# Kernel optimization log

Measured on AMD Instinct MI355X. Metric: run time of the kernel, lower is better.

Reference implementation:

```python
import jax, jax.numpy as jnp
import numpy as np

N = 50000   # nodes
E = 800000  # directed edges
D = 128     # input_channels


def _kaiming(key, shape):
    fan_in = shape[0]
    return jax.random.normal(key, shape, jnp.float32) * np.float32(np.sqrt(2.0 / fan_in))


def setup_inputs():
    key = jax.random.key(0)
    ks = jax.random.split(key, 8)
    x = jax.random.normal(ks[0], (N, D), jnp.float32)
    edge_index = jax.random.randint(ks[1], (2, E), 0, N, dtype=jnp.int32)
    return {
        "x": x,
        "edge_index": edge_index,
        "W_in": _kaiming(ks[2], (D, D)),      "b_in": jnp.zeros((D,), jnp.float32),
        "W1": _kaiming(ks[3], (D, 2 * D)),    "b1": jnp.zeros((2 * D,), jnp.float32),
        "W2": _kaiming(ks[4], (2 * D, D)),    "b2": jnp.zeros((D,), jnp.float32),
        "W3": _kaiming(ks[5], (D, D // 2)),   "b3": jnp.zeros((D // 2,), jnp.float32),
        "W_out": _kaiming(ks[6], (D // 2, 1)), "b_out": jnp.zeros((1,), jnp.float32),
    }


def _gcn_conv(x, src, dst, W, b, n):
    """PyG GCNConv: add self-loops, symmetric D^-1/2 (A+I) D^-1/2 normalization."""
    h = x @ W  # [n, out]
    loop = jnp.arange(n, dtype=src.dtype)
    s = jnp.concatenate([src, loop])  # message sources (x_j)
    d = jnp.concatenate([dst, loop])  # aggregation targets (x_i)
    deg = jax.ops.segment_sum(jnp.ones_like(d, jnp.float32), d, num_segments=n)
    dis = jnp.where(deg > 0, jax.lax.rsqrt(jnp.maximum(deg, 1.0)), 0.0)
    norm = dis[s] * dis[d]  # [E+n]
    msg = h[s] * norm[:, None]  # gather + scale
    out = jax.ops.segment_sum(msg, d, num_segments=n)  # scatter-add
    return out + b


def reference(x, edge_index, W_in, b_in, W1, b1, W2, b2, W3, b3, W_out, b_out):
    src, dst = edge_index[0], edge_index[1]
    n = x.shape[0]
    lrelu = lambda t: jax.nn.leaky_relu(t, 0.01)
    # dropout in eval mode (identity)
    h = lrelu(x @ W_in + b_in)
    h = lrelu(_gcn_conv(h, src, dst, W1, b1, n))
    h = lrelu(_gcn_conv(h, src, dst, W2, b2, n))
    h = lrelu(_gcn_conv(h, src, dst, W3, b3, n))
    return h @ W_out + b_out  # [n, 1]
```

## Files before the change

### kernel.cpp

```cpp
#include <hip/hip_runtime.h>


#define LRELU(v) ((v) > 0.f ? (v) : 0.01f * (v))

typedef __attribute__((ext_vector_type(8))) _Float16 half8;
typedef __attribute__((ext_vector_type(8))) float float8;
typedef __attribute__((ext_vector_type(4))) float floatx4;

constexpr int CAP = 64;

__global__ __launch_bounds__(256) void k_prep(const int* __restrict__ src,
                                              const int* __restrict__ dst,
                                              int* __restrict__ cnt,
                                              unsigned short* __restrict__ pad,
                                              const float* __restrict__ W_in,
                                              const float* __restrict__ W1,
                                              const float* __restrict__ W2,
                                              const float* __restrict__ W3,
                                              _Float16* __restrict__ wt_in,
                                              _Float16* __restrict__ wt1,
                                              _Float16* __restrict__ wt2,
                                              _Float16* __restrict__ wt3,
                                              int E, int PR) {
  const int b = blockIdx.x;
  const int tid = threadIdx.x;
  if (b < 128) {
    const int m = b >> 5;
    const int blk = b & 31;
    const int idx = blk * 256 + tid;
    if (m == 0) {
      for (int i = idx; i < 128 * 128; i += 8192) {
        const int k = i >> 7, f = i & 127;
        wt_in[f * 128 + k] = (_Float16)W_in[i];
      }
    } else if (m == 1) {
      for (int i = idx; i < 128 * 256; i += 8192) {
        const int k = i >> 8, f = i & 255;
        wt1[f * 128 + k] = (_Float16)W1[i];
      }
    } else if (m == 2) {
      for (int i = idx; i < 256 * 128; i += 8192) {
        const int k = i >> 7, f = i & 127;
        wt2[f * 256 + k] = (_Float16)W2[i];
      }
    } else {
      for (int i = idx; i < 128 * 64; i += 8192) {
        const int k = i >> 6, f = i & 63;
        wt3[f * 128 + k] = (_Float16)W3[i];
      }
    }
  } else {
    const int bb = b - 128;
    const int range = bb & 7;
    const int chunk = bb >> 3;
    const int e = chunk * 256 + tid;
    if (e < E) {
      const int d = dst[e];
      if (d / PR == range) {
        const int pos = atomicAdd(&cnt[d], 1);
        if (pos < CAP) pad[(long)d * CAP + pos] = (unsigned short)src[e];
      }
    }
  }
}

template <int K, int F, int EPI, typename IT>
__global__ __launch_bounds__(256) void k_gemm(const IT* __restrict__ X,
                                              const _Float16* __restrict__ Wt,
                                              const float* __restrict__ b,
                                              const int* __restrict__ cnt,
                                              _Float16* __restrict__ out, int M) {
  constexpr int TM = 64;
  constexpr int PAD = 8;
  constexpr int LK = K + PAD;
  constexpr int CW = F / 4;
  constexpr int NT = CW / 16;
  constexpr int NK = K / 32;
  __shared__ _Float16 xs[TM * LK];

  const int m0 = blockIdx.x * TM;
  const int tid = threadIdx.x;
  const int w = tid >> 6;
  const int lane = tid & 63;
  const int m = lane & 15;
  const int q = lane >> 4;

  half8 breg[NT][NK];
#pragma unroll
  for (int t = 0; t < NT; ++t)
#pragma unroll
    for (int kc = 0; kc < NK; ++kc)
      breg[t][kc] =
          *(const half8*)&Wt[(long)(w * CW + t * 16 + m) * K + kc * 32 + q * 8];

  constexpr int CPR = K / 8;
  for (int idx = tid; idx < TM * CPR; idx += 256) {
    const int row = idx / CPR;
    const int kk = idx % CPR;
    const int g = m0 + row;
    half8 h = (half8)(_Float16)0.f;
    if (g < M) {
      if constexpr (sizeof(IT) == 4) {
        const float4* p = (const float4*)&X[(long)g * K + kk * 8];
        float4 a = p[0], c = p[1];
        h[0] = (_Float16)a.x; h[1] = (_Float16)a.y;
        h[2] = (_Float16)a.z; h[3] = (_Float16)a.w;
        h[4] = (_Float16)c.x; h[5] = (_Float16)c.y;
        h[6] = (_Float16)c.z; h[7] = (_Float16)c.w;
      } else {
        h = *(const half8*)&X[(long)g * K + kk * 8];
      }
    }
    *(half8*)&xs[row * LK + kk * 8] = h;
  }
  __syncthreads();

  floatx4 acc[4][NT];
#pragma unroll
  for (int rt = 0; rt < 4; ++rt)
#pragma unroll
    for (int t = 0; t < NT; ++t) acc[rt][t] = (floatx4){0.f, 0.f, 0.f, 0.f};

#pragma unroll
  for (int kc = 0; kc < NK; ++kc) {
    half8 af[4];
#pragma unroll
    for (int rt = 0; rt < 4; ++rt)
      af[rt] = *(const half8*)&xs[(rt * 16 + m) * LK + kc * 32 + q * 8];
#pragma unroll
    for (int rt = 0; rt < 4; ++rt)
#pragma unroll
      for (int t = 0; t < NT; ++t)
        acc[rt][t] = __builtin_amdgcn_mfma_f32_16x16x32_f16(af[rt], breg[t][kc],
                                                            acc[rt][t], 0, 0, 0);
  }

#pragma unroll
  for (int rt = 0; rt < 4; ++rt) {
#pragma unroll
    for (int r = 0; r < 4; ++r) {
      const int row = m0 + rt * 16 + q * 4 + r;
      if (row < M) {
        const float dv = rsqrtf((float)cnt[row] + 1.0f);
#pragma unroll
        for (int t = 0; t < NT; ++t) {
          const int col = w * CW + t * 16 + m;
          float v = acc[rt][t][r];
          if constexpr (EPI == 0) { v += b[col]; v = LRELU(v); v *= dv; }
          if constexpr (EPI == 2) { v *= dv; }
          out[(long)row * F + col] = (_Float16)v;
        }
      }
    }
  }
}

__global__ __launch_bounds__(256) void k_gemm2x(const _Float16* __restrict__ X,
                                                const _Float16* __restrict__ Wt1,
                                                const float* __restrict__ b1,
                                                const _Float16* __restrict__ Wt2,
                                                const int* __restrict__ cnt,
                                                _Float16* __restrict__ out,
                                                int M) {
  constexpr int TM = 64;
  constexpr int LK1 = 128 + 8;
  constexpr int LK2 = 256 + 8;
  __shared__ _Float16 xs[TM * LK1];
  __shared__ _Float16 ys[TM * LK2];

  const int m0 = blockIdx.x * TM;
  const int tid = threadIdx.x;
  const int w = tid >> 6;
  const int lane = tid & 63;
  const int m = lane & 15;
  const int q = lane >> 4;

  for (int idx = tid; idx < TM * 16; idx += 256) {
    const int row = idx >> 4;
    const int kk = idx & 15;
    const int g = m0 + row;
    half8 h = (half8)(_Float16)0.f;
    if (g < M) h = *(const half8*)&X[(long)g * 128 + kk * 8];
    *(half8*)&xs[row * LK1 + kk * 8] = h;
  }

  half8 breg1[4][4];
#pragma unroll
  for (int t = 0; t < 4; ++t)
#pragma unroll
    for (int kc = 0; kc < 4; ++kc)
      breg1[t][kc] =
          *(const half8*)&Wt1[(long)(w * 64 + t * 16 + m) * 128 + kc * 32 + q * 8];

  __syncthreads();

  floatx4 acc1[4][4];
#pragma unroll
  for (int rt = 0; rt < 4; ++rt)
#pragma unroll
    for (int t = 0; t < 4; ++t) acc1[rt][t] = (floatx4){0.f, 0.f, 0.f, 0.f};

#pragma unroll
  for (int kc = 0; kc < 4; ++kc) {
    half8 af[4];
#pragma unroll
    for (int rt = 0; rt < 4; ++rt)
      af[rt] = *(const half8*)&xs[(rt * 16 + m) * LK1 + kc * 32 + q * 8];
#pragma unroll
    for (int rt = 0; rt < 4; ++rt)
#pragma unroll
      for (int t = 0; t < 4; ++t)
        acc1[rt][t] = __builtin_amdgcn_mfma_f32_16x16x32_f16(af[rt], breg1[t][kc],
                                                             acc1[rt][t], 0, 0, 0);
  }

#pragma unroll
  for (int rt = 0; rt < 4; ++rt) {
#pragma unroll
    for (int r = 0; r < 4; ++r) {
      const int row = rt * 16 + q * 4 + r;
#pragma unroll
      for (int t = 0; t < 4; ++t) {
        const int col = w * 64 + t * 16 + m;
        float v = acc1[rt][t][r] + b1[col];
        ys[row * LK2 + col] = (_Float16)LRELU(v);
      }
    }
  }

  half8 breg2[2][8];
#pragma unroll
  for (int t = 0; t < 2; ++t)
#pragma unroll
    for (int kc = 0; kc < 8; ++kc)
      breg2[t][kc] =
          *(const half8*)&Wt2[(long)(w * 32 + t * 16 + m) * 256 + kc * 32 + q * 8];

  __syncthreads();

  floatx4 acc2[4][2];
#pragma unroll
  for (int rt = 0; rt < 4; ++rt)
#pragma unroll
    for (int t = 0; t < 2; ++t) acc2[rt][t] = (floatx4){0.f, 0.f, 0.f, 0.f};

#pragma unroll
  for (int kc = 0; kc < 8; ++kc) {
    half8 af[4];
#pragma unroll
    for (int rt = 0; rt < 4; ++rt)
      af[rt] = *(const half8*)&ys[(rt * 16 + m) * LK2 + kc * 32 + q * 8];
#pragma unroll
    for (int rt = 0; rt < 4; ++rt)
#pragma unroll
      for (int t = 0; t < 2; ++t)
        acc2[rt][t] = __builtin_amdgcn_mfma_f32_16x16x32_f16(af[rt], breg2[t][kc],
                                                             acc2[rt][t], 0, 0, 0);
  }

#pragma unroll
  for (int rt = 0; rt < 4; ++rt) {
#pragma unroll
    for (int r = 0; r < 4; ++r) {
      const int row = m0 + rt * 16 + q * 4 + r;
      if (row < M) {
        const float dv = rsqrtf((float)cnt[row] + 1.0f);
#pragma unroll
        for (int t = 0; t < 2; ++t) {
          const int col = w * 32 + t * 16 + m;
          out[(long)row * 128 + col] = (_Float16)(acc2[rt][t][r] * dv);
        }
      }
    }
  }
}

template <int F, int MODE>
__global__ __launch_bounds__(256) void k_agg(const _Float16* __restrict__ G,
                                             const unsigned short* __restrict__ pad,
                                             const int* __restrict__ cnt,
                                             const float* __restrict__ b,
                                             const float* __restrict__ Wout,
                                             const float* __restrict__ bout,
                                             void* __restrict__ out, int N) {
  const int w = threadIdx.x >> 6;
  const int lane = threadIdx.x & 63;
  const int c = lane & 7;
  const int j = lane >> 3;
  const int n = j >> 2;
  const int jj = j & 3;
  const int i0 = blockIdx.x * 8 + w * 2;
  int i = i0 + n;
  const bool valid = (i < N);
  if (!valid) i = N - 1;
  const int col0 = (F == 128) ? ((int)blockIdx.y << 6) : 0;

  const _Float16* gbase = G + col0 + c * 8;
  const int cn = min(cnt[i], CAP);
  const unsigned short* plist = pad + (long)i * CAP;

  float8 acc = {0.f, 0.f, 0.f, 0.f, 0.f, 0.f, 0.f, 0.f};
  if (jj == 0)
    acc = __builtin_convertvector(*(const half8*)(gbase + (long)i * F), float8);
  for (int e = jj; e < cn; e += 4) {
    const int s = plist[e];
    acc += __builtin_convertvector(*(const half8*)(gbase + (long)s * F), float8);
  }
#pragma unroll
  for (int k = 0; k < 8; ++k) {
    acc[k] += __shfl_xor(acc[k], 8);
    acc[k] += __shfl_xor(acc[k], 16);
  }

  const float dv = rsqrtf((float)cnt[i] + 1.0f);
  if constexpr (MODE == 2) {
    float p = 0.f;
#pragma unroll
    for (int k = 0; k < 8; ++k) {
      const int col = c * 8 + k;
      float v = acc[k] * dv + b[col];
      v = LRELU(v);
      p += v * Wout[col];
    }
    p += __shfl_xor(p, 1);
    p += __shfl_xor(p, 2);
    p += __shfl_xor(p, 4);
    if (valid && jj == 0 && c == 0) ((float*)out)[i] = p + bout[0];
  } else {
    if (valid && jj == 0) {
      half8 hv;
#pragma unroll
      for (int k = 0; k < 8; ++k) {
        float v = acc[k] * dv;
        if constexpr (MODE == 1) { v += b[col0 + c * 8 + k]; v = LRELU(v); }
        hv[k] = (_Float16)v;
      }
      *(half8*)&((_Float16*)out)[(long)i * F + col0 + c * 8] = hv;
    }
  }
}


extern "C" void kernel_launch(void* const* d_in, const int* in_sizes, int n_in,
                              void* d_out, int out_size, void* d_ws, size_t ws_size,
                              hipStream_t stream) {
  const float* x     = (const float*)d_in[0];
  const int* eidx    = (const int*)d_in[1];
  const float* W_in  = (const float*)d_in[2];
  const float* b_in  = (const float*)d_in[3];
  const float* W1    = (const float*)d_in[4];
  const float* b1    = (const float*)d_in[5];
  const float* W2    = (const float*)d_in[6];
  const float* b2    = (const float*)d_in[7];
  const float* W3    = (const float*)d_in[8];
  const float* b3    = (const float*)d_in[9];
  const float* W_out = (const float*)d_in[10];
  const float* b_out = (const float*)d_in[11];
  float* out = (float*)d_out;

  const int N = in_sizes[0] / 128;
  const int E = in_sizes[1] / 2;
  const int* src = eidx;
  const int* dst = eidx + E;
  const int PR = (N + 7) / 8;

  size_t off = 0;
  char* base = (char*)d_ws;
  auto alloc = [&](size_t bytes) -> void* {
    void* p = base + off;
    off = (off + bytes + 255) & ~(size_t)255;
    return p;
  };
  int* cnt            = (int*)alloc((size_t)N * sizeof(int));
  unsigned short* pad = (unsigned short*)alloc((size_t)N * CAP * 2);
  _Float16* wt_in     = (_Float16*)alloc((size_t)128 * 128 * 2);
  _Float16* wt1       = (_Float16*)alloc((size_t)256 * 128 * 2);
  _Float16* wt2       = (_Float16*)alloc((size_t)128 * 256 * 2);
  _Float16* wt3       = (_Float16*)alloc((size_t)64 * 128 * 2);
  _Float16* buf1      = (_Float16*)alloc((size_t)N * 128 * 2);
  _Float16* buf2      = (_Float16*)alloc((size_t)N * 128 * 2);
  _Float16* buf3      = (_Float16*)alloc((size_t)N * 64 * 2);

  hipMemsetAsync(cnt, 0, (size_t)N * sizeof(int), stream);

  const int gE = (E + 255) / 256;
  const int gRows = (N + 63) / 64;
  const int gAggP = (N + 7) / 8;

  k_prep<<<128 + 8 * gE, 256, 0, stream>>>(src, dst, cnt, pad,
                                           W_in, W1, W2, W3,
                                           wt_in, wt1, wt2, wt3, E, PR);

  k_gemm<128, 128, 0, float><<<gRows, 256, 0, stream>>>(x, wt_in, b_in, cnt,
                                                        buf1, N);
  k_agg<128, 0><<<dim3(gAggP, 2), 256, 0, stream>>>(buf1, pad, cnt, nullptr,
                                                    nullptr, nullptr, buf2, N);
  k_gemm2x<<<gRows, 256, 0, stream>>>(buf2, wt1, b1, wt2, cnt, buf1, N);
  k_agg<128, 1><<<dim3(gAggP, 2), 256, 0, stream>>>(buf1, pad, cnt, b2,
                                                    nullptr, nullptr, buf2, N);
  k_gemm<128, 64, 2, _Float16><<<gRows, 256, 0, stream>>>(buf2, wt3, nullptr,
                                                          cnt, buf3, N);
  k_agg<64, 2><<<gAggP, 256, 0, stream>>>(buf3, pad, cnt, b3,
                                          W_out, b_out, out, N);
}
```

Before: 273.8 us.

## Fuse all GCN stages into one persistent cooperative kernel with grid syncs

Replaces the memset and seven separate kernel launches with a single cooperative persistent kernel that loops over tiles and separates the phases with grid-wide barriers. Weight conversion, count zeroing, edge bucketing, the GEMMs and the aggregations all run inside it, and the old multi-kernel path stays as a fallback. The aim is to remove launch gaps and tail effects between the small stages. In exchange, the grid is capped by occupancy, which limits latency hiding in the gather-bound aggregation, grid.sync adds its own cost, and gemm2x now reuses one shared buffer with an extra barrier.

```diff
diff --git a/kernel.cpp b/kernel.cpp
--- a/kernel.cpp
+++ b/kernel.cpp
@@ -1,4 +1,7 @@
 #include <hip/hip_runtime.h>
+#include <hip/hip_cooperative_groups.h>
+
+namespace cg = cooperative_groups;
 
 
 #define LRELU(v) ((v) > 0.f ? (v) : 0.01f * (v))
@@ -8,6 +11,360 @@
 typedef __attribute__((ext_vector_type(4))) float floatx4;
 
 constexpr int CAP = 64;
+constexpr int SMEM_H = 16896;
+
+template <int K, int F, int EPI, typename IT>
+__device__ void phase_gemm(const IT* __restrict__ X,
+                           const _Float16* __restrict__ Wt,
+                           const float* __restrict__ b,
+                           const int* __restrict__ cnt,
+                           _Float16* __restrict__ out, int M,
+                           _Float16* xs) {
+  constexpr int TM = 64;
+  constexpr int LK = K + 8;
+  constexpr int CW = F / 4;
+  constexpr int NT = CW / 16;
+  constexpr int NK = K / 32;
+
+  const int tid = threadIdx.x;
+  const int w = tid >> 6;
+  const int lane = tid & 63;
+  const int m = lane & 15;
+  const int q = lane >> 4;
+  const int nTiles = (M + TM - 1) / TM;
+
+  half8 breg[NT][NK];
+#pragma unroll
+  for (int t = 0; t < NT; ++t)
+#pragma unroll
+    for (int kc = 0; kc < NK; ++kc)
+      breg[t][kc] =
+          *(const half8*)&Wt[(long)(w * CW + t * 16 + m) * K + kc * 32 + q * 8];
+
+  for (int tile = blockIdx.x; tile < nTiles; tile += gridDim.x) {
+    const int m0 = tile * TM;
+    __syncthreads();
+    constexpr int CPR = K / 8;
+    for (int idx = tid; idx < TM * CPR; idx += 256) {
+      const int row = idx / CPR;
+      const int kk = idx % CPR;
+      const int g = m0 + row;
+      half8 h = (half8)(_Float16)0.f;
+      if (g < M) {
+        if constexpr (sizeof(IT) == 4) {
+          const float4* p = (const float4*)&X[(long)g * K + kk * 8];
+          float4 a = p[0], c = p[1];
+          h[0] = (_Float16)a.x; h[1] = (_Float16)a.y;
+          h[2] = (_Float16)a.z; h[3] = (_Float16)a.w;
+          h[4] = (_Float16)c.x; h[5] = (_Float16)c.y;
+          h[6] = (_Float16)c.z; h[7] = (_Float16)c.w;
+        } else {
+          h = *(const half8*)&X[(long)g * K + kk * 8];
+        }
+      }
+      *(half8*)&xs[row * LK + kk * 8] = h;
+    }
+    __syncthreads();
+
+    floatx4 acc[4][NT];
+#pragma unroll
+    for (int rt = 0; rt < 4; ++rt)
+#pragma unroll
+      for (int t = 0; t < NT; ++t) acc[rt][t] = (floatx4){0.f, 0.f, 0.f, 0.f};
+
+#pragma unroll
+    for (int kc = 0; kc < NK; ++kc) {
+      half8 af[4];
+#pragma unroll
+      for (int rt = 0; rt < 4; ++rt)
+        af[rt] = *(const half8*)&xs[(rt * 16 + m) * LK + kc * 32 + q * 8];
+#pragma unroll
+      for (int rt = 0; rt < 4; ++rt)
+#pragma unroll
+        for (int t = 0; t < NT; ++t)
+          acc[rt][t] = __builtin_amdgcn_mfma_f32_16x16x32_f16(
+              af[rt], breg[t][kc], acc[rt][t], 0, 0, 0);
+    }
+
+#pragma unroll
+    for (int rt = 0; rt < 4; ++rt) {
+#pragma unroll
+      for (int r = 0; r < 4; ++r) {
+        const int row = m0 + rt * 16 + q * 4 + r;
+        if (row < M) {
+          const float dv = rsqrtf((float)cnt[row] + 1.0f);
+#pragma unroll
+          for (int t = 0; t < NT; ++t) {
+            const int col = w * CW + t * 16 + m;
+            float v = acc[rt][t][r];
+            if constexpr (EPI == 0) { v += b[col]; v = LRELU(v); v *= dv; }
+            if constexpr (EPI == 2) { v *= dv; }
+            out[(long)row * F + col] = (_Float16)v;
+          }
+        }
+      }
+    }
+  }
+}
+
+__device__ void phase_gemm2x(const _Float16* __restrict__ X,
+                             const _Float16* __restrict__ Wt1,
+                             const float* __restrict__ b1,
+                             const _Float16* __restrict__ Wt2,
+                             const int* __restrict__ cnt,
+                             _Float16* __restrict__ out, int M,
+                             _Float16* smem) {
+  constexpr int TM = 64;
+  constexpr int LK1 = 128 + 8;
+  constexpr int LK2 = 256 + 8;
+  _Float16* xs = smem;
+  _Float16* ys = smem;
+
+  const int tid = threadIdx.x;
+  const int w = tid >> 6;
+  const int lane = tid & 63;
+  const int m = lane & 15;
+  const int q = lane >> 4;
+  const int nTiles = (M + TM - 1) / TM;
+
+  half8 breg1[4][4];
+#pragma unroll
+  for (int t = 0; t < 4; ++t)
+#pragma unroll
+    for (int kc = 0; kc < 4; ++kc)
+      breg1[t][kc] = *(const half8*)&Wt1[(long)(w * 64 + t * 16 + m) * 128 +
+                                         kc * 32 + q * 8];
+  half8 breg2[2][8];
+#pragma unroll
+  for (int t = 0; t < 2; ++t)
+#pragma unroll
+    for (int kc = 0; kc < 8; ++kc)
+      breg2[t][kc] = *(const half8*)&Wt2[(long)(w * 32 + t * 16 + m) * 256 +
+                                         kc * 32 + q * 8];
+
+  for (int tile = blockIdx.x; tile < nTiles; tile += gridDim.x) {
+    const int m0 = tile * TM;
+    __syncthreads();
+    for (int idx = tid; idx < TM * 16; idx += 256) {
+      const int row = idx >> 4;
+      const int kk = idx & 15;
+      const int g = m0 + row;
+      half8 h = (half8)(_Float16)0.f;
+      if (g < M) h = *(const half8*)&X[(long)g * 128 + kk * 8];
+      *(half8*)&xs[row * LK1 + kk * 8] = h;
+    }
+    __syncthreads();
+
+    floatx4 acc1[4][4];
+#pragma unroll
+    for (int rt = 0; rt < 4; ++rt)
+#pragma unroll
+      for (int t = 0; t < 4; ++t) acc1[rt][t] = (floatx4){0.f, 0.f, 0.f, 0.f};
+
+#pragma unroll
+    for (int kc = 0; kc < 4; ++kc) {
+      half8 af[4];
+#pragma unroll
+      for (int rt = 0; rt < 4; ++rt)
+        af[rt] = *(const half8*)&xs[(rt * 16 + m) * LK1 + kc * 32 + q * 8];
+#pragma unroll
+      for (int rt = 0; rt < 4; ++rt)
+#pragma unroll
+        for (int t = 0; t < 4; ++t)
+          acc1[rt][t] = __builtin_amdgcn_mfma_f32_16x16x32_f16(
+              af[rt], breg1[t][kc], acc1[rt][t], 0, 0, 0);
+    }
+    __syncthreads();
+
+#pragma unroll
+    for (int rt = 0; rt < 4; ++rt) {
+#pragma unroll
+      for (int r = 0; r < 4; ++r) {
+        const int row = rt * 16 + q * 4 + r;
+#pragma unroll
+        for (int t = 0; t < 4; ++t) {
+          const int col = w * 64 + t * 16 + m;
+          float v = acc1[rt][t][r] + b1[col];
+          ys[row * LK2 + col] = (_Float16)LRELU(v);
+        }
+      }
+    }
+    __syncthreads();
+
+    floatx4 acc2[4][2];
+#pragma unroll
+    for (int rt = 0; rt < 4; ++rt)
+#pragma unroll
+      for (int t = 0; t < 2; ++t) acc2[rt][t] = (floatx4){0.f, 0.f, 0.f, 0.f};
+
+#pragma unroll
+    for (int kc = 0; kc < 8; ++kc) {
+      half8 af[4];
+#pragma unroll
+      for (int rt = 0; rt < 4; ++rt)
+        af[rt] = *(const half8*)&ys[(rt * 16 + m) * LK2 + kc * 32 + q * 8];
+#pragma unroll
+      for (int rt = 0; rt < 4; ++rt)
+#pragma unroll
+        for (int t = 0; t < 2; ++t)
+          acc2[rt][t] = __builtin_amdgcn_mfma_f32_16x16x32_f16(
+              af[rt], breg2[t][kc], acc2[rt][t], 0, 0, 0);
+    }
+
+#pragma unroll
+    for (int rt = 0; rt < 4; ++rt) {
+#pragma unroll
+      for (int r = 0; r < 4; ++r) {
+        const int row = m0 + rt * 16 + q * 4 + r;
+        if (row < M) {
+          const float dv = rsqrtf((float)cnt[row] + 1.0f);
+#pragma unroll
+          for (int t = 0; t < 2; ++t) {
+            const int col = w * 32 + t * 16 + m;
+            out[(long)row * 128 + col] = (_Float16)(acc2[rt][t][r] * dv);
+          }
+        }
+      }
+    }
+  }
+}
+
+template <int F, int MODE>
+__device__ void phase_agg(const _Float16* __restrict__ G,
+                          const unsigned short* __restrict__ pad,
+                          const int* __restrict__ cnt,
+                          const float* __restrict__ b,
+                          const float* __restrict__ Wout,
+                          const float* __restrict__ bout,
+                          void* __restrict__ out, int N) {
+  const int w = threadIdx.x >> 6;
+  const int lane = threadIdx.x & 63;
+  const int c = lane & 7;
+  const int j = lane >> 3;
+  const int n = j >> 2;
+  const int jj = j & 3;
+  const int uBlk = (N + 7) / 8;
+  const int nUnits = (F == 128) ? 2 * uBlk : uBlk;
+
+  for (int u = blockIdx.x; u < nUnits; u += gridDim.x) {
+    const int y = (F == 128) ? (u / uBlk) : 0;
+    const int ub = (F == 128) ? (u % uBlk) : u;
+    int i = ub * 8 + w * 2 + n;
+    const bool valid = (i < N);
+    if (!valid) i = N - 1;
+    const int col0 = y << 6;
+
+    const _Float16* gbase = G + col0 + c * 8;
+    const int cn = min(cnt[i], CAP);
+    const unsigned short* plist = pad + (long)i * CAP;
+
+    float8 acc = {0.f, 0.f, 0.f, 0.f, 0.f, 0.f, 0.f, 0.f};
+    if (jj == 0)
+      acc = __builtin_convertvector(*(const half8*)(gbase + (long)i * F), float8);
+    for (int e = jj; e < cn; e += 4) {
+      const int s = plist[e];
+      acc += __builtin_convertvector(*(const half8*)(gbase + (long)s * F), float8);
+    }
+#pragma unroll
+    for (int k = 0; k < 8; ++k) {
+      acc[k] += __shfl_xor(acc[k], 8);
+      acc[k] += __shfl_xor(acc[k], 16);
+    }
+
+    const float dv = rsqrtf((float)cnt[i] + 1.0f);
+    if constexpr (MODE == 2) {
+      float p = 0.f;
+#pragma unroll
+      for (int k = 0; k < 8; ++k) {
+        const int col = c * 8 + k;
+        float v = acc[k] * dv + b[col];
+        v = LRELU(v);
+        p += v * Wout[col];
+      }
+      p += __shfl_xor(p, 1);
+      p += __shfl_xor(p, 2);
+      p += __shfl_xor(p, 4);
+      if (valid && jj == 0 && c == 0) ((float*)out)[i] = p + bout[0];
+    } else {
+      if (valid && jj == 0) {
+        half8 hv;
+#pragma unroll
+        for (int k = 0; k < 8; ++k) {
+          float v = acc[k] * dv;
+          if constexpr (MODE == 1) { v += b[col0 + c * 8 + k]; v = LRELU(v); }
+          hv[k] = (_Float16)v;
+        }
+        *(half8*)&((_Float16*)out)[(long)i * F + col0 + c * 8] = hv;
+      }
+    }
+  }
+}
+
+__global__ __launch_bounds__(256, 2) void k_mega(
+    const float* __restrict__ x, const int* __restrict__ src,
+    const int* __restrict__ dst, const float* __restrict__ W_in,
+    const float* __restrict__ b_in, const float* __restrict__ W1,
+    const float* __restrict__ b1, const float* __restrict__ W2,
+    const float* __restrict__ b2, const float* __restrict__ W3,
+    const float* __restrict__ b3, const float* __restrict__ W_out,
+    const float* __restrict__ b_out, int* __restrict__ cnt,
+    unsigned short* __restrict__ pad, _Float16* __restrict__ wt_in,
+    _Float16* __restrict__ wt1, _Float16* __restrict__ wt2,
+    _Float16* __restrict__ wt3, _Float16* __restrict__ buf1,
+    _Float16* __restrict__ buf2, _Float16* __restrict__ buf3,
+    float* __restrict__ out, int N, int E, int PR) {
+  cg::grid_group grid = cg::this_grid();
+  __shared__ _Float16 smem[SMEM_H];
+
+  const int tid = threadIdx.x;
+  const int b = blockIdx.x;
+  const int gid = b * 256 + tid;
+  const int GS = gridDim.x * 256;
+
+  for (int i = gid; i < N; i += GS) cnt[i] = 0;
+  for (int i = gid; i < 128 * 128; i += GS) {
+    const int k = i >> 7, f = i & 127;
+    wt_in[f * 128 + k] = (_Float16)W_in[i];
+  }
+  for (int i = gid; i < 128 * 256; i += GS) {
+    const int k = i >> 8, f = i & 255;
+    wt1[f * 128 + k] = (_Float16)W1[i];
+  }
+  for (int i = gid; i < 256 * 128; i += GS) {
+    const int k = i >> 7, f = i & 127;
+    wt2[f * 256 + k] = (_Float16)W2[i];
+  }
+  for (int i = gid; i < 128 * 64; i += GS) {
+    const int k = i >> 6, f = i & 63;
+    wt3[f * 128 + k] = (_Float16)W3[i];
+  }
+  grid.sync();
+
+  {
+    const int range = b & 7;
+    const int stride = (gridDim.x >> 3) * 256;
+    for (int e = (b >> 3) * 256 + tid; e < E; e += stride) {
+      const int d = dst[e];
+      if (d / PR == range) {
+        const int pos = atomicAdd(&cnt[d], 1);
+        if (pos < CAP) pad[(long)d * CAP + pos] = (unsigned short)src[e];
+      }
+    }
+  }
+  grid.sync();
+
+  phase_gemm<128, 128, 0, float>(x, wt_in, b_in, cnt, buf1, N, smem);
+  grid.sync();
+  phase_agg<128, 0>(buf1, pad, cnt, nullptr, nullptr, nullptr, buf2, N);
+  grid.sync();
+  phase_gemm2x(buf2, wt1, b1, wt2, cnt, buf1, N, smem);
+  grid.sync();
+  phase_agg<128, 1>(buf1, pad, cnt, b2, nullptr, nullptr, buf2, N);
+  grid.sync();
+  phase_gemm<128, 64, 2, _Float16>(buf2, wt3, nullptr, cnt, buf3, N, smem);
+  grid.sync();
+  phase_agg<64, 2>(buf3, pad, cnt, b3, W_out, b_out, out, N);
+}
 
 __global__ __launch_bounds__(256) void k_prep(const int* __restrict__ src,
                                               const int* __restrict__ dst,
@@ -26,8 +383,7 @@
   const int tid = threadIdx.x;
   if (b < 128) {
     const int m = b >> 5;
-    const int blk = b & 31;
-    const int idx = blk * 256 + tid;
+    const int idx = (b & 31) * 256 + tid;
     if (m == 0) {
       for (int i = idx; i < 128 * 128; i += 8192) {
         const int k = i >> 7, f = i & 127;
@@ -52,8 +408,7 @@
   } else {
     const int bb = b - 128;
     const int range = bb & 7;
-    const int chunk = bb >> 3;
-    const int e = chunk * 256 + tid;
+    const int e = (bb >> 3) * 256 + tid;
     if (e < E) {
       const int d = dst[e];
       if (d / PR == range) {
@@ -70,89 +425,8 @@
                                               const float* __restrict__ b,
                                               const int* __restrict__ cnt,
                                               _Float16* __restrict__ out, int M) {
-  constexpr int TM = 64;
-  constexpr int PAD = 8;
-  constexpr int LK = K + PAD;
-  constexpr int CW = F / 4;
-  constexpr int NT = CW / 16;
-  constexpr int NK = K / 32;
-  __shared__ _Float16 xs[TM * LK];
-
-  const int m0 = blockIdx.x * TM;
-  const int tid = threadIdx.x;
-  const int w = tid >> 6;
-  const int lane = tid & 63;
-  const int m = lane & 15;
-  const int q = lane >> 4;
-
-  half8 breg[NT][NK];
-#pragma unroll
-  for (int t = 0; t < NT; ++t)
-#pragma unroll
-    for (int kc = 0; kc < NK; ++kc)
-      breg[t][kc] =
-          *(const half8*)&Wt[(long)(w * CW + t * 16 + m) * K + kc * 32 + q * 8];
-
-  constexpr int CPR = K / 8;
-  for (int idx = tid; idx < TM * CPR; idx += 256) {
-    const int row = idx / CPR;
-    const int kk = idx % CPR;
-    const int g = m0 + row;
-    half8 h = (half8)(_Float16)0.f;
-    if (g < M) {
-      if constexpr (sizeof(IT) == 4) {
-        const float4* p = (const float4*)&X[(long)g * K + kk * 8];
-        float4 a = p[0], c = p[1];
-        h[0] = (_Float16)a.x; h[1] = (_Float16)a.y;
-        h[2] = (_Float16)a.z; h[3] = (_Float16)a.w;
-        h[4] = (_Float16)c.x; h[5] = (_Float16)c.y;
-        h[6] = (_Float16)c.z; h[7] = (_Float16)c.w;
-      } else {
-        h = *(const half8*)&X[(long)g * K + kk * 8];
-      }
-    }
-    *(half8*)&xs[row * LK + kk * 8] = h;
-  }
-  __syncthreads();
-
-  floatx4 acc[4][NT];
-#pragma unroll
-  for (int rt = 0; rt < 4; ++rt)
-#pragma unroll
-    for (int t = 0; t < NT; ++t) acc[rt][t] = (floatx4){0.f, 0.f, 0.f, 0.f};
-
-#pragma unroll
-  for (int kc = 0; kc < NK; ++kc) {
-    half8 af[4];
-#pragma unroll
-    for (int rt = 0; rt < 4; ++rt)
-      af[rt] = *(const half8*)&xs[(rt * 16 + m) * LK + kc * 32 + q * 8];
-#pragma unroll
-    for (int rt = 0; rt < 4; ++rt)
-#pragma unroll
-      for (int t = 0; t < NT; ++t)
-        acc[rt][t] = __builtin_amdgcn_mfma_f32_16x16x32_f16(af[rt], breg[t][kc],
-                                                            acc[rt][t], 0, 0, 0);
-  }
-
-#pragma unroll
-  for (int rt = 0; rt < 4; ++rt) {
-#pragma unroll
-    for (int r = 0; r < 4; ++r) {
-      const int row = m0 + rt * 16 + q * 4 + r;
-      if (row < M) {
-        const float dv = rsqrtf((float)cnt[row] + 1.0f);
-#pragma unroll
-        for (int t = 0; t < NT; ++t) {
-          const int col = w * CW + t * 16 + m;
-          float v = acc[rt][t][r];
-          if constexpr (EPI == 0) { v += b[col]; v = LRELU(v); v *= dv; }
-          if constexpr (EPI == 2) { v *= dv; }
-          out[(long)row * F + col] = (_Float16)v;
-        }
-      }
-    }
-  }
+  __shared__ _Float16 smem[64 * (K + 8)];
+  phase_gemm<K, F, EPI, IT>(X, Wt, b, cnt, out, M, smem);
 }
 
 __global__ __launch_bounds__(256) void k_gemm2x(const _Float16* __restrict__ X,
@@ -162,117 +436,8 @@
                                                 const int* __restrict__ cnt,
                                                 _Float16* __restrict__ out,
                                                 int M) {
-  constexpr int TM = 64;
-  constexpr int LK1 = 128 + 8;
-  constexpr int LK2 = 256 + 8;
-  __shared__ _Float16 xs[TM * LK1];
-  __shared__ _Float16 ys[TM * LK2];
-
-  const int m0 = blockIdx.x * TM;
-  const int tid = threadIdx.x;
-  const int w = tid >> 6;
-  const int lane = tid & 63;
-  const int m = lane & 15;
-  const int q = lane >> 4;
-
-  for (int idx = tid; idx < TM * 16; idx += 256) {
-    const int row = idx >> 4;
-    const int kk = idx & 15;
-    const int g = m0 + row;
-    half8 h = (half8)(_Float16)0.f;
-    if (g < M) h = *(const half8*)&X[(long)g * 128 + kk * 8];
-    *(half8*)&xs[row * LK1 + kk * 8] = h;
-  }
-
-  half8 breg1[4][4];
-#pragma unroll
-  for (int t = 0; t < 4; ++t)
-#pragma unroll
-    for (int kc = 0; kc < 4; ++kc)
-      breg1[t][kc] =
-          *(const half8*)&Wt1[(long)(w * 64 + t * 16 + m) * 128 + kc * 32 + q * 8];
-
-  __syncthreads();
-
-  floatx4 acc1[4][4];
-#pragma unroll
-  for (int rt = 0; rt < 4; ++rt)
-#pragma unroll
-    for (int t = 0; t < 4; ++t) acc1[rt][t] = (floatx4){0.f, 0.f, 0.f, 0.f};
-
-#pragma unroll
-  for (int kc = 0; kc < 4; ++kc) {
-    half8 af[4];
-#pragma unroll
-    for (int rt = 0; rt < 4; ++rt)
-      af[rt] = *(const half8*)&xs[(rt * 16 + m) * LK1 + kc * 32 + q * 8];
-#pragma unroll
-    for (int rt = 0; rt < 4; ++rt)
-#pragma unroll
-      for (int t = 0; t < 4; ++t)
-        acc1[rt][t] = __builtin_amdgcn_mfma_f32_16x16x32_f16(af[rt], breg1[t][kc],
-                                                             acc1[rt][t], 0, 0, 0);
-  }
-
-#pragma unroll
-  for (int rt = 0; rt < 4; ++rt) {
-#pragma unroll
-    for (int r = 0; r < 4; ++r) {
-      const int row = rt * 16 + q * 4 + r;
-#pragma unroll
-      for (int t = 0; t < 4; ++t) {
-        const int col = w * 64 + t * 16 + m;
-        float v = acc1[rt][t][r] + b1[col];
-        ys[row * LK2 + col] = (_Float16)LRELU(v);
-      }
-    }
-  }
-
-  half8 breg2[2][8];
-#pragma unroll
-  for (int t = 0; t < 2; ++t)
-#pragma unroll
-    for (int kc = 0; kc < 8; ++kc)
-      breg2[t][kc] =
-          *(const half8*)&Wt2[(long)(w * 32 + t * 16 + m) * 256 + kc * 32 + q * 8];
-
-  __syncthreads();
-
-  floatx4 acc2[4][2];
-#pragma unroll
-  for (int rt = 0; rt < 4; ++rt)
-#pragma unroll
-    for (int t = 0; t < 2; ++t) acc2[rt][t] = (floatx4){0.f, 0.f, 0.f, 0.f};
-
-#pragma unroll
-  for (int kc = 0; kc < 8; ++kc) {
-    half8 af[4];
-#pragma unroll
-    for (int rt = 0; rt < 4; ++rt)
-      af[rt] = *(const half8*)&ys[(rt * 16 + m) * LK2 + kc * 32 + q * 8];
-#pragma unroll
-    for (int rt = 0; rt < 4; ++rt)
-#pragma unroll
-      for (int t = 0; t < 2; ++t)
-        acc2[rt][t] = __builtin_amdgcn_mfma_f32_16x16x32_f16(af[rt], breg2[t][kc],
-                                                             acc2[rt][t], 0, 0, 0);
-  }
-
-#pragma unroll
-  for (int rt = 0; rt < 4; ++rt) {
-#pragma unroll
-    for (int r = 0; r < 4; ++r) {
-      const int row = m0 + rt * 16 + q * 4 + r;
-      if (row < M) {
-        const float dv = rsqrtf((float)cnt[row] + 1.0f);
-#pragma unroll
-        for (int t = 0; t < 2; ++t) {
-          const int col = w * 32 + t * 16 + m;
-          out[(long)row * 128 + col] = (_Float16)(acc2[rt][t][r] * dv);
-        }
-      }
-    }
-  }
+  __shared__ _Float16 smem[SMEM_H];
+  phase_gemm2x(X, Wt1, b1, Wt2, cnt, out, M, smem);
 }
 
 template <int F, int MODE>
@@ -283,61 +448,7 @@
                                              const float* __restrict__ Wout,
                                              const float* __restrict__ bout,
                                              void* __restrict__ out, int N) {
-  const int w = threadIdx.x >> 6;
-  const int lane = threadIdx.x & 63;
-  const int c = lane & 7;
-  const int j = lane >> 3;
-  const int n = j >> 2;
-  const int jj = j & 3;
-  const int i0 = blockIdx.x * 8 + w * 2;
-  int i = i0 + n;
-  const bool valid = (i < N);
-  if (!valid) i = N - 1;
-  const int col0 = (F == 128) ? ((int)blockIdx.y << 6) : 0;
-
-  const _Float16* gbase = G + col0 + c * 8;
-  const int cn = min(cnt[i], CAP);
-  const unsigned short* plist = pad + (long)i * CAP;
-
-  float8 acc = {0.f, 0.f, 0.f, 0.f, 0.f, 0.f, 0.f, 0.f};
-  if (jj == 0)
-    acc = __builtin_convertvector(*(const half8*)(gbase + (long)i * F), float8);
-  for (int e = jj; e < cn; e += 4) {
-    const int s = plist[e];
-    acc += __builtin_convertvector(*(const half8*)(gbase + (long)s * F), float8);
-  }
-#pragma unroll
-  for (int k = 0; k < 8; ++k) {
-    acc[k] += __shfl_xor(acc[k], 8);
-    acc[k] += __shfl_xor(acc[k], 16);
-  }
-
-  const float dv = rsqrtf((float)cnt[i] + 1.0f);
-  if constexpr (MODE == 2) {
-    float p = 0.f;
-#pragma unroll
-    for (int k = 0; k < 8; ++k) {
-      const int col = c * 8 + k;
-      float v = acc[k] * dv + b[col];
-      v = LRELU(v);
-      p += v * Wout[col];
-    }
-    p += __shfl_xor(p, 1);
-    p += __shfl_xor(p, 2);
-    p += __shfl_xor(p, 4);
-    if (valid && jj == 0 && c == 0) ((float*)out)[i] = p + bout[0];
-  } else {
-    if (valid && jj == 0) {
-      half8 hv;
-#pragma unroll
-      for (int k = 0; k < 8; ++k) {
-        float v = acc[k] * dv;
-        if constexpr (MODE == 1) { v += b[col0 + c * 8 + k]; v = LRELU(v); }
-        hv[k] = (_Float16)v;
-      }
-      *(half8*)&((_Float16*)out)[(long)i * F + col0 + c * 8] = hv;
-    }
-  }
+  phase_agg<F, MODE>(G, pad, cnt, b, Wout, bout, out, N);
 }
 
 
@@ -358,11 +469,11 @@
   const float* b_out = (const float*)d_in[11];
   float* out = (float*)d_out;
 
-  const int N = in_sizes[0] / 128;
-  const int E = in_sizes[1] / 2;
+  int N = in_sizes[0] / 128;
+  int E = in_sizes[1] / 2;
   const int* src = eidx;
   const int* dst = eidx + E;
-  const int PR = (N + 7) / 8;
+  int PR = (N + 7) / 8;
 
   size_t off = 0;
   char* base = (char*)d_ws;
@@ -381,25 +492,49 @@
   _Float16* buf2      = (_Float16*)alloc((size_t)N * 128 * 2);
   _Float16* buf3      = (_Float16*)alloc((size_t)N * 64 * 2);
 
-  hipMemsetAsync(cnt, 0, (size_t)N * sizeof(int), stream);
-
-  const int gE = (E + 255) / 256;
-  const int gRows = (N + 63) / 64;
-  const int gAggP = (N + 7) / 8;
-
-  k_prep<<<128 + 8 * gE, 256, 0, stream>>>(src, dst, cnt, pad,
-                                           W_in, W1, W2, W3,
-                                           wt_in, wt1, wt2, wt3, E, PR);
-
-  k_gemm<128, 128, 0, float><<<gRows, 256, 0, stream>>>(x, wt_in, b_in, cnt,
-                                                        buf1, N);
-  k_agg<128, 0><<<dim3(gAggP, 2), 256, 0, stream>>>(buf1, pad, cnt, nullptr,
-                                                    nullptr, nullptr, buf2, N);
-  k_gemm2x<<<gRows, 256, 0, stream>>>(buf2, wt1, b1, wt2, cnt, buf1, N);
-  k_agg<128, 1><<<dim3(gAggP, 2), 256, 0, stream>>>(buf1, pad, cnt, b2,
-                                                    nullptr, nullptr, buf2, N);
-  k_gemm<128, 64, 2, _Float16><<<gRows, 256, 0, stream>>>(buf2, wt3, nullptr,
-                                                          cnt, buf3, N);
-  k_agg<64, 2><<<gAggP, 256, 0, stream>>>(buf3, pad, cnt, b3,
-                                          W_out, b_out, out, N);
-}
+  int dev = 0;
+  hipGetDevice(&dev);
+  int numCU = 0;
+  hipDeviceGetAttribute(&numCU, hipDeviceAttributeMultiprocessorCount, dev);
+  int maxB = 0;
+  hipError_t qe = hipOccupancyMaxActiveBlocksPerMultiprocessor(
+      &maxB, (const void*)k_mega, 256, 0);
+  int grid = (qe == hipSuccess && numCU > 0) ? maxB * numCU : 0;
+  grid &= ~7;
+  if (grid > 2048) grid = 2048;
+
+  bool coop = (grid >= 8);
+  if (coop) {
+    void* kargs[] = {
+        (void*)&x,     (void*)&src,  (void*)&dst,  (void*)&W_in,
+        (void*)&b_in,  (void*)&W1,   (void*)&b1,   (void*)&W2,
+        (void*)&b2,    (void*)&W3,   (void*)&b3,   (void*)&W_out,
+        (void*)&b_out, (void*)&cnt,  (void*)&pad,  (void*)&wt_in,
+        (void*)&wt1,   (void*)&wt2,  (void*)&wt3,  (void*)&buf1,
+        (void*)&buf2,  (void*)&buf3, (void*)&out,  (void*)&N,
+        (void*)&E,     (void*)&PR};
+    hipError_t le = hipLaunchCooperativeKernel((const void*)k_mega, dim3(grid),
+                                               dim3(256), kargs, 0, stream);
+    coop = (le == hipSuccess);
+  }
+
+  if (!coop) {
+    const int gE = (E + 255) / 256;
+    const int gRows = (N + 63) / 64;
+    const int gAggP = (N + 7) / 8;
+    hipMemsetAsync(cnt, 0, (size_t)N * sizeof(int), stream);
+    k_prep<<<128 + 8 * gE, 256, 0, stream>>>(src, dst, cnt, pad, W_in, W1, W2,
+                                             W3, wt_in, wt1, wt2, wt3, E, PR);
+    k_gemm<128, 128, 0, float><<<gRows, 256, 0, stream>>>(x, wt_in, b_in, cnt,
+                                                          buf1, N);
+    k_agg<128, 0><<<2 * gAggP, 256, 0, stream>>>(buf1, pad, cnt, nullptr,
+                                                 nullptr, nullptr, buf2, N);
+    k_gemm2x<<<gRows, 256, 0, stream>>>(buf2, wt1, b1, wt2, cnt, buf1, N);
+    k_agg<128, 1><<<2 * gAggP, 256, 0, stream>>>(buf1, pad, cnt, b2, nullptr,
+                                                 nullptr, buf2, N);
+    k_gemm<128, 64, 2, _Float16><<<gRows, 256, 0, stream>>>(buf2, wt3, nullptr,
+                                                            cnt, buf3, N);
+    k_agg<64, 2><<<gAggP, 256, 0, stream>>>(buf3, pad, cnt, b3, W_out, b_out,
+                                            out, N);
+  }
+}
```

New measurement: 327.1 us. 1.19x slower.
